# Kernel tuning notes

Measured on AMD Instinct MI355X. Metric: run time of the kernel, lower is better.

The kernel has to match this reference:

```python
import jax, jax.numpy as jnp
import numpy as np
from jax import lax
from jax.scipy.stats import norm

KERNLEN = 31
NSIG = 4
EPS = 1e-3


def _gkern(kernlen=KERNLEN, nsig=NSIG):
    # Faithful port of HA._gkern (scipy.stats.norm.cdf -> jax.scipy.stats.norm.cdf)
    interval = (2.0 * nsig + 1.0) / kernlen
    x = jnp.linspace(-nsig - interval / 2.0, nsig + interval / 2.0, kernlen + 1)
    kern1d = jnp.diff(norm.cdf(x))
    kernel_raw = jnp.sqrt(jnp.outer(kern1d, kern1d))
    kernel = kernel_raw / kernel_raw.sum()
    return kernel.astype(jnp.float32)


def setup_inputs() -> dict:
    key = jax.random.key(0)
    attention = jax.random.uniform(key, (64, 1, 512, 512), dtype=jnp.float32)
    gaussian_kernel = _gkern()[None, None, :, :]  # OIHW [1,1,31,31]
    return {"attention": attention, "gaussian_kernel": gaussian_kernel}


def reference(attention, gaussian_kernel):
    a = jnp.clip(attention, 0.0, 1.0)
    # single-channel 31x31 conv, 'same' padding (pad 15)
    soft = lax.conv_general_dilated(
        a, gaussian_kernel,
        window_strides=(1, 1),
        padding=[(15, 15), (15, 15)],
        dimension_numbers=("NCHW", "OIHW", "NCHW"),
    )
    # per-image min-max normalization over H,W (per (n,c) slice)
    mx = soft.max(axis=(2, 3), keepdims=True)
    mn = soft.min(axis=(2, 3), keepdims=True)
    soft = (soft - mn) / jnp.maximum(mx - mn, EPS)  # torch.clamp(max-min, min=eps)
    soft = jnp.nan_to_num(soft, nan=0.0, posinf=1.0, neginf=0.0)
    return jnp.maximum(soft, a)
```

## Files before the change

kernel.cpp:

```cpp
#include <hip/hip_runtime.h>
#include <math.h>
#include <stdint.h>

#define IMGS 64
#define HWDIM 512
#define KLEN 31
#define RAD 15
#define EPSV 1e-3f
#define MM_STRIDE 32
#define RSLOT 25


typedef __attribute__((address_space(3))) uint8_t  lds_u8;
typedef const __attribute__((address_space(1))) uint8_t g_u8;

__global__ __launch_bounds__(128) void init_k(const float* __restrict__ gk,
                                              float* __restrict__ w,
                                              int* __restrict__ mm) {
    int t = threadIdx.x;
    if (t < KLEN) w[t] = sqrtf(gk[t * KLEN + t]);
    if (t < IMGS) { mm[t * MM_STRIDE] = 0x7F800000; mm[t * MM_STRIDE + 1] = 0; }
}

template <bool EDGE>
__device__ __forceinline__ void conv_body(const float* __restrict__ attn,
                                          float* __restrict__ out,
                                          const float* __restrict__ wg,
                                          int* __restrict__ mm,
                                          int img, int x0, int y0,
                                          float* __restrict__ raw,
                                          float* __restrict__ sred) {
    const int t = threadIdx.x;
    const float* src = attn + ((size_t)img << 18);
    const int gbq = (x0 >> 2) - 4;

#pragma unroll
    for (int it = 0; it < 10; ++it) {
        const int idx = t + (it << 8);
        if (idx < 94 * RSLOT) {
            int r = idx / RSLOT;
            int s = idx - r * RSLOT;
            if (s == 24) s = 0;
            int y = y0 - RAD + r;
            y = y < 0 ? 0 : (y > HWDIM - 1 ? HWDIM - 1 : y);
            int g = gbq + s;
            if (EDGE) g = g < 0 ? 0 : (g > 127 ? 127 : g);
            const float* gp = src + ((size_t)y << 9) + (g << 2);
            __builtin_amdgcn_global_load_lds((g_u8*)gp, (lds_u8*)&raw[idx << 2],
                                             16, 0, 0);
        }
    }
    __syncthreads();

#pragma unroll
    for (int rnd = 0; rnd < 2; ++rnd) {
        const int i = t + (rnd << 8);
        if (i < 94 * 4) {
            const int r = i >> 2, q = i & 3;
            const float* rb = &raw[(r * RSLOT + (q << 2)) << 2];
            float4 b[12];
#pragma unroll
            for (int m = 0; m < 12; ++m) b[m] = *(const float4*)(rb + (m << 2));
            const int y = y0 - RAD + r;
            const bool vy = !EDGE || ((unsigned)y < HWDIM);
            const int gb = gbq + (q << 2);
            float vv[48];
#pragma unroll
            for (int m = 0; m < 12; ++m) {
                const bool vx = !EDGE || (vy && ((unsigned)(gb + m) < 128u));
                vv[4 * m + 0] = vx ? fminf(fmaxf(b[m].x, 0.f), 1.f) : 0.f;
                vv[4 * m + 1] = vx ? fminf(fmaxf(b[m].y, 0.f), 1.f) : 0.f;
                vv[4 * m + 2] = vx ? fminf(fmaxf(b[m].z, 0.f), 1.f) : 0.f;
                vv[4 * m + 3] = vx ? fminf(fmaxf(b[m].w, 0.f), 1.f) : 0.f;
            }
            float* dst = &raw[(r * RSLOT + 4 + (q << 2)) << 2];
#pragma unroll
            for (int d = 0; d < 4; ++d) {
                float4 o;
                float* op = &o.x;
#pragma unroll
                for (int s = 0; s < 4; ++s) {
                    const int oc = (d << 2) + s;
                    float a = 0.f;
#pragma unroll
                    for (int k = 0; k < KLEN; ++k) a += vv[oc + 1 + k] * wg[k];
                    op[s] = a;
                }
                *(float4*)(dst + (d << 2)) = o;
            }
        }
    }
    __syncthreads();

    const int tx = t & 15;
    const int ty = t >> 4;
    float4 acc[4];
#pragma unroll
    for (int i = 0; i < 4; ++i) acc[i] = make_float4(0.f, 0.f, 0.f, 0.f);
#pragma unroll
    for (int k = 0; k < 34; ++k) {
        const float4 v =
            *(const float4*)&raw[(((ty << 2) + k) * RSLOT + 4 + tx) << 2];
#pragma unroll
        for (int i = 0; i < 4; ++i) {
            const int j = k - i;
            if (j >= 0 && j < KLEN) {
                const float w = wg[j];
                acc[i].x += v.x * w;
                acc[i].y += v.y * w;
                acc[i].z += v.z * w;
                acc[i].w += v.w * w;
            }
        }
    }
    float* dst = out + ((size_t)img << 18);
    float lmin = INFINITY, lmax = -INFINITY;
#pragma unroll
    for (int i = 0; i < 4; ++i) {
        *(float4*)&dst[(size_t)(y0 + (ty << 2) + i) * HWDIM + x0 + (tx << 2)] = acc[i];
        lmin = fminf(lmin, fminf(fminf(acc[i].x, acc[i].y), fminf(acc[i].z, acc[i].w)));
        lmax = fmaxf(lmax, fmaxf(fmaxf(acc[i].x, acc[i].y), fmaxf(acc[i].z, acc[i].w)));
    }
#pragma unroll
    for (int off = 1; off < 64; off <<= 1) {
        lmin = fminf(lmin, __shfl_xor(lmin, off, 64));
        lmax = fmaxf(lmax, __shfl_xor(lmax, off, 64));
    }
    const int lane = t & 63, wid = t >> 6;
    if (lane == 0) { sred[wid] = lmin; sred[4 + wid] = lmax; }
    __syncthreads();
    if (t == 0) {
        float bmin = fminf(fminf(sred[0], sred[1]), fminf(sred[2], sred[3]));
        float bmax = fmaxf(fmaxf(sred[4], sred[5]), fmaxf(sred[6], sred[7]));
        atomicMin(&mm[img * MM_STRIDE], __float_as_int(bmin));
        atomicMax(&mm[img * MM_STRIDE + 1], __float_as_int(bmax));
    }
}

__global__ __launch_bounds__(256) void conv_k(const float* __restrict__ attn,
                                              float* __restrict__ out,
                                              const float* __restrict__ wg,
                                              int* __restrict__ mm) {
    __shared__ float raw[94 * RSLOT * 4];
    __shared__ float sred[8];
    const int sw  = ((blockIdx.x & 7) << 9) + (blockIdx.x >> 3);
    const int img = sw >> 6;
    const int by  = (sw >> 3) & 7;
    const int bx  = sw & 7;
    const int x0 = bx << 6;
    const int y0 = by << 6;
    if (bx == 0 || bx == 7 || by == 0 || by == 7)
        conv_body<true>(attn, out, wg, mm, img, x0, y0, raw, sred);
    else
        conv_body<false>(attn, out, wg, mm, img, x0, y0, raw, sred);
}

__global__ __launch_bounds__(256) void final_k(const float* __restrict__ attn,
                                               float* __restrict__ out,
                                               const int* __restrict__ mm) {
    const int img = blockIdx.x >> 6;
    const float mn = __int_as_float(mm[img * MM_STRIDE]);
    const float mx = __int_as_float(mm[img * MM_STRIDE + 1]);
    const float inv = 1.0f / fmaxf(mx - mn, EPSV);
    const size_t base0 = ((size_t)blockIdx.x << 12) + ((size_t)threadIdx.x << 2);
#pragma unroll
    for (int h = 0; h < 4; ++h) {
        const size_t base = base0 + (size_t)h * 1024;
        float4 s = *(const float4*)(out + base);
        float4 a = *(const float4*)(attn + base);
        float4 o;
        o.x = fmaxf((s.x - mn) * inv, fminf(fmaxf(a.x, 0.f), 1.f));
        o.y = fmaxf((s.y - mn) * inv, fminf(fmaxf(a.y, 0.f), 1.f));
        o.z = fmaxf((s.z - mn) * inv, fminf(fmaxf(a.z, 0.f), 1.f));
        o.w = fmaxf((s.w - mn) * inv, fminf(fmaxf(a.w, 0.f), 1.f));
        *(float4*)(out + base) = o;
    }
}

extern "C" void kernel_launch(void* const* d_in, const int* in_sizes, int n_in,
                              void* d_out, int out_size, void* d_ws, size_t ws_size,
                              hipStream_t stream) {
    const float* attn = (const float*)d_in[0];
    const float* gk   = (const float*)d_in[1];
    float* out  = (float*)d_out;
    float* wsf  = (float*)d_ws;
    float* w1d  = wsf;
    int*   mm   = (int*)(wsf + 32);

    init_k<<<1, 128, 0, stream>>>(gk, w1d, mm);
    conv_k<<<4096, 256, 0, stream>>>(attn, out, w1d, mm);
    final_k<<<IMGS * HWDIM * HWDIM / 4096, 256, 0, stream>>>(attn, out, mm);
}
```

Before: 81.05 us.

## Use single-wave 64x32 tiles with register sliding-window vertical convolution

```diff
diff --git a/kernel.cpp b/kernel.cpp
--- a/kernel.cpp
+++ b/kernel.cpp
@@ -28,50 +28,51 @@
                                           const float* __restrict__ wg,
                                           int* __restrict__ mm,
                                           int img, int x0, int y0,
-                                          float* __restrict__ raw,
-                                          float* __restrict__ sred) {
-    const int t = threadIdx.x;
+                                          float* __restrict__ raw) {
+    const int lane = threadIdx.x;
     const float* src = attn + ((size_t)img << 18);
     const int gbq = (x0 >> 2) - 4;
 
 #pragma unroll
-    for (int it = 0; it < 10; ++it) {
-        const int idx = t + (it << 8);
-        if (idx < 94 * RSLOT) {
-            int r = idx / RSLOT;
-            int s = idx - r * RSLOT;
-            if (s == 24) s = 0;
-            int y = y0 - RAD + r;
-            y = y < 0 ? 0 : (y > HWDIM - 1 ? HWDIM - 1 : y);
-            int g = gbq + s;
-            if (EDGE) g = g < 0 ? 0 : (g > 127 ? 127 : g);
-            const float* gp = src + ((size_t)y << 9) + (g << 2);
-            __builtin_amdgcn_global_load_lds((g_u8*)gp, (lds_u8*)&raw[idx << 2],
-                                             16, 0, 0);
-        }
+    for (int i = 0; i < 25; ++i) {
+        const int idx = (i << 6) + lane;
+        int r = idx / 25;
+        r = r > 61 ? 61 : r;
+        int s = idx - r * 25;
+        s = s > 24 ? 24 : s;
+        if (s == 24) s = 23;
+        int y = y0 - RAD + r;
+        y = y < 0 ? 0 : (y > HWDIM - 1 ? HWDIM - 1 : y);
+        int g = gbq + s;
+        if (EDGE) g = g < 0 ? 0 : (g > 127 ? 127 : g);
+        const float* gp = src + ((size_t)y << 9) + (g << 2);
+        __builtin_amdgcn_global_load_lds((g_u8*)gp, (lds_u8*)&raw[idx << 2],
+                                         16, 0, 0);
     }
-    __syncthreads();
+    __builtin_amdgcn_sched_barrier(0);
+    asm volatile("s_waitcnt vmcnt(0)" ::: "memory");
+    __builtin_amdgcn_sched_barrier(0);
 
 #pragma unroll
-    for (int rnd = 0; rnd < 2; ++rnd) {
-        const int i = t + (rnd << 8);
-        if (i < 94 * 4) {
-            const int r = i >> 2, q = i & 3;
+    for (int rnd = 0; rnd < 4; ++rnd) {
+        const int r = (rnd << 4) + (lane >> 2);
+        const int q = lane & 3;
+        if (r < 62) {
             const float* rb = &raw[(r * RSLOT + (q << 2)) << 2];
-            float4 b[12];
+            float4 bv[12];
 #pragma unroll
-            for (int m = 0; m < 12; ++m) b[m] = *(const float4*)(rb + (m << 2));
+            for (int m = 0; m < 12; ++m) bv[m] = *(const float4*)(rb + (m << 2));
             const int y = y0 - RAD + r;
-            const bool vy = !EDGE || ((unsigned)y < HWDIM);
+            const bool vy = (unsigned)y < (unsigned)HWDIM;
             const int gb = gbq + (q << 2);
             float vv[48];
 #pragma unroll
             for (int m = 0; m < 12; ++m) {
-                const bool vx = !EDGE || (vy && ((unsigned)(gb + m) < 128u));
-                vv[4 * m + 0] = vx ? fminf(fmaxf(b[m].x, 0.f), 1.f) : 0.f;
-                vv[4 * m + 1] = vx ? fminf(fmaxf(b[m].y, 0.f), 1.f) : 0.f;
-                vv[4 * m + 2] = vx ? fminf(fmaxf(b[m].z, 0.f), 1.f) : 0.f;
-                vv[4 * m + 3] = vx ? fminf(fmaxf(b[m].w, 0.f), 1.f) : 0.f;
+                const bool vx = !EDGE || ((unsigned)(gb + m) < 128u);
+                vv[4 * m + 0] = vx ? fminf(fmaxf(bv[m].x, 0.f), 1.f) : 0.f;
+                vv[4 * m + 1] = vx ? fminf(fmaxf(bv[m].y, 0.f), 1.f) : 0.f;
+                vv[4 * m + 2] = vx ? fminf(fmaxf(bv[m].z, 0.f), 1.f) : 0.f;
+                vv[4 * m + 3] = vx ? fminf(fmaxf(bv[m].w, 0.f), 1.f) : 0.f;
             }
             float* dst = &raw[(r * RSLOT + 4 + (q << 2)) << 2];
 #pragma unroll
@@ -79,80 +80,62 @@
                 float4 o;
                 float* op = &o.x;
 #pragma unroll
-                for (int s = 0; s < 4; ++s) {
-                    const int oc = (d << 2) + s;
+                for (int s2 = 0; s2 < 4; ++s2) {
+                    const int oc = (d << 2) + s2;
                     float a = 0.f;
 #pragma unroll
                     for (int k = 0; k < KLEN; ++k) a += vv[oc + 1 + k] * wg[k];
-                    op[s] = a;
+                    op[s2] = a;
                 }
+                if (!vy) o = make_float4(0.f, 0.f, 0.f, 0.f);
                 *(float4*)(dst + (d << 2)) = o;
             }
         }
     }
-    __syncthreads();
 
-    const int tx = t & 15;
-    const int ty = t >> 4;
-    float4 acc[4];
+    float win[62];
 #pragma unroll
-    for (int i = 0; i < 4; ++i) acc[i] = make_float4(0.f, 0.f, 0.f, 0.f);
-#pragma unroll
-    for (int k = 0; k < 34; ++k) {
-        const float4 v =
-            *(const float4*)&raw[(((ty << 2) + k) * RSLOT + 4 + tx) << 2];
-#pragma unroll
-        for (int i = 0; i < 4; ++i) {
-            const int j = k - i;
-            if (j >= 0 && j < KLEN) {
-                const float w = wg[j];
-                acc[i].x += v.x * w;
-                acc[i].y += v.y * w;
-                acc[i].z += v.z * w;
-                acc[i].w += v.w * w;
-            }
-        }
-    }
-    float* dst = out + ((size_t)img << 18);
+    for (int k = 0; k < 62; ++k)
+        win[k] = raw[k * (RSLOT * 4) + 16 + lane];
+    float* dst = out + ((size_t)img << 18) + ((size_t)y0 << 9) + x0 + lane;
     float lmin = INFINITY, lmax = -INFINITY;
 #pragma unroll
-    for (int i = 0; i < 4; ++i) {
-        *(float4*)&dst[(size_t)(y0 + (ty << 2) + i) * HWDIM + x0 + (tx << 2)] = acc[i];
-        lmin = fminf(lmin, fminf(fminf(acc[i].x, acc[i].y), fminf(acc[i].z, acc[i].w)));
-        lmax = fmaxf(lmax, fmaxf(fmaxf(acc[i].x, acc[i].y), fmaxf(acc[i].z, acc[i].w)));
+    for (int i = 0; i < 32; ++i) {
+        float a = 0.f;
+#pragma unroll
+        for (int k = 0; k < KLEN; ++k) a += win[i + k] * wg[k];
+        dst[(size_t)i << 9] = a;
+        lmin = fminf(lmin, a);
+        lmax = fmaxf(lmax, a);
     }
 #pragma unroll
     for (int off = 1; off < 64; off <<= 1) {
         lmin = fminf(lmin, __shfl_xor(lmin, off, 64));
         lmax = fmaxf(lmax, __shfl_xor(lmax, off, 64));
     }
-    const int lane = t & 63, wid = t >> 6;
-    if (lane == 0) { sred[wid] = lmin; sred[4 + wid] = lmax; }
-    __syncthreads();
-    if (t == 0) {
-        float bmin = fminf(fminf(sred[0], sred[1]), fminf(sred[2], sred[3]));
-        float bmax = fmaxf(fmaxf(sred[4], sred[5]), fmaxf(sred[6], sred[7]));
-        atomicMin(&mm[img * MM_STRIDE], __float_as_int(bmin));
-        atomicMax(&mm[img * MM_STRIDE + 1], __float_as_int(bmax));
+    if (lane == 0) {
+        atomicMin(&mm[img * MM_STRIDE], __float_as_int(lmin));
+        atomicMax(&mm[img * MM_STRIDE + 1], __float_as_int(lmax));
     }
 }
 
-__global__ __launch_bounds__(256) void conv_k(const float* __restrict__ attn,
-                                              float* __restrict__ out,
-                                              const float* __restrict__ wg,
-                                              int* __restrict__ mm) {
-    __shared__ float raw[94 * RSLOT * 4];
-    __shared__ float sred[8];
-    const int sw  = ((blockIdx.x & 7) << 9) + (blockIdx.x >> 3);
-    const int img = sw >> 6;
-    const int by  = (sw >> 3) & 7;
-    const int bx  = sw & 7;
+__global__ __launch_bounds__(64) void conv_k(const float* __restrict__ attn,
+                                             float* __restrict__ out,
+                                             const float* __restrict__ wg,
+                                             int* __restrict__ mm) {
+    __shared__ float raw[1600 * 4];
+    const int b   = blockIdx.x;
+    const int sw  = ((b & 7) << 10) | (b >> 3);
+    const int img = sw >> 7;
+    const int s   = sw & 127;
+    const int by  = s >> 3;
+    const int bx  = s & 7;
     const int x0 = bx << 6;
-    const int y0 = by << 6;
-    if (bx == 0 || bx == 7 || by == 0 || by == 7)
-        conv_body<true>(attn, out, wg, mm, img, x0, y0, raw, sred);
+    const int y0 = by << 5;
+    if (bx == 0 || bx == 7)
+        conv_body<true>(attn, out, wg, mm, img, x0, y0, raw);
     else
-        conv_body<false>(attn, out, wg, mm, img, x0, y0, raw, sred);
+        conv_body<false>(attn, out, wg, mm, img, x0, y0, raw);
 }
 
 __global__ __launch_bounds__(256) void final_k(const float* __restrict__ attn,
@@ -188,6 +171,6 @@
     int*   mm   = (int*)(wsf + 32);
 
     init_k<<<1, 128, 0, stream>>>(gk, w1d, mm);
-    conv_k<<<4096, 256, 0, stream>>>(attn, out, w1d, mm);
+    conv_k<<<IMGS * 128, 64, 0, stream>>>(attn, out, w1d, mm);
     final_k<<<IMGS * HWDIM * HWDIM / 4096, 256, 0, stream>>>(attn, out, mm);
 }
```

New measurement: 122.3 us. 50.9% more time.
